# Performance work log

Measured on AMD Instinct MI355X. Metric: run time of the kernel, lower is better.

Reference implementation:

```python
import jax, jax.numpy as jnp
import numpy as np

D_MODEL = 768
NUM_HEADS = 12
D_K = D_MODEL // NUM_HEADS
D_FF = 3072
EPS = 1e-5


def _layer_norm(x, gamma, beta):
    mu = jnp.mean(x, axis=-1, keepdims=True)
    var = jnp.mean(jnp.square(x - mu), axis=-1, keepdims=True)
    return (x - mu) * jax.lax.rsqrt(var + EPS) * gamma + beta


def setup_inputs() -> dict:
    key = jax.random.key(0)
    ks = jax.random.split(key, 16)
    s = 1.0 / np.sqrt(D_MODEL)
    sf = 1.0 / np.sqrt(D_FF)
    inp = {
        "x": jax.random.normal(ks[0], (2, 2048, D_MODEL), dtype=jnp.float32),
        "Wq": jax.random.uniform(ks[1], (D_MODEL, D_MODEL), jnp.float32, -s, s),
        "bq": jax.random.uniform(ks[2], (D_MODEL,), jnp.float32, -s, s),
        "Wk": jax.random.uniform(ks[3], (D_MODEL, D_MODEL), jnp.float32, -s, s),
        "bk": jax.random.uniform(ks[4], (D_MODEL,), jnp.float32, -s, s),
        "Wv": jax.random.uniform(ks[5], (D_MODEL, D_MODEL), jnp.float32, -s, s),
        "bv": jax.random.uniform(ks[6], (D_MODEL,), jnp.float32, -s, s),
        "Wo": jax.random.uniform(ks[7], (D_MODEL, D_MODEL), jnp.float32, -s, s),
        "bo": jax.random.uniform(ks[8], (D_MODEL,), jnp.float32, -s, s),
        "W1": jax.random.uniform(ks[9], (D_MODEL, D_FF), jnp.float32, -s, s),
        "b1": jax.random.uniform(ks[10], (D_FF,), jnp.float32, -s, s),
        "W2": jax.random.uniform(ks[11], (D_FF, D_MODEL), jnp.float32, -sf, sf),
        "b2": jax.random.uniform(ks[12], (D_MODEL,), jnp.float32, -sf, sf),
        "g1": jnp.ones((D_MODEL,), jnp.float32),
        "be1": jnp.zeros((D_MODEL,), jnp.float32),
        "g2": jnp.ones((D_MODEL,), jnp.float32),
        "be2": jnp.zeros((D_MODEL,), jnp.float32),
    }
    return inp


def reference(x, Wq, bq, Wk, bk, Wv, bv, Wo, bo, W1, b1, W2, b2, g1, be1, g2, be2):
    B, S, _ = x.shape

    def split(h):  # (B,S,D) -> (B,H,S,Dk)
        return h.reshape(B, S, NUM_HEADS, D_K).transpose(0, 2, 1, 3)

    q = split(x @ Wq + bq)
    k = split(x @ Wk + bk)
    v = split(x @ Wv + bv)

    # naive attention: materialize full (B,H,S,S) scores as in the original
    scores = jnp.einsum("bhsd,bhtd->bhst", q, k) / np.sqrt(D_K)
    attn = jax.nn.softmax(scores, axis=-1)
    ctx = jnp.einsum("bhst,bhtd->bhsd", attn, v)
    ctx = ctx.transpose(0, 2, 1, 3).reshape(B, S, D_MODEL)
    attn_out = ctx @ Wo + bo

    x = _layer_norm(x + attn_out, g1, be1)
    ff = jax.nn.relu(x @ W1 + b1) @ W2 + b2
    x = _layer_norm(x + ff, g2, be2)
    return x
```

## Files before the change

kernel.cpp:

```cpp
#include <hip/hip_runtime.h>
#include <cstdint>


typedef unsigned short u16;
typedef unsigned int u32;
typedef __attribute__((ext_vector_type(4))) float f32x4;
typedef __attribute__((ext_vector_type(8))) short s16x8;
typedef __attribute__((ext_vector_type(4))) u16  u16x4;
typedef __attribute__((ext_vector_type(2))) u32  u32x2;

#define AS1 __attribute__((address_space(1)))
#define AS3 __attribute__((address_space(3)))

__device__ __forceinline__ u16 f2b(float f) {
  union { float f; unsigned u; } v; v.f = f;
  unsigned r = v.u + 0x7FFFu + ((v.u >> 16) & 1u);
  return (u16)(r >> 16);
}

__device__ __forceinline__ float b2f(u16 v) {
  union { float f; u32 u; } x; x.u = ((u32)v) << 16; return x.f;
}

__device__ __forceinline__ void gl_lds16(const void* g, void* lds_uniform_base) {
  __builtin_amdgcn_global_load_lds((const AS1 void*)g, (AS3 void*)lds_uniform_base, 16, 0, 0);
}

__device__ __forceinline__ f32x4 mfma16(s16x8 a, s16x8 b, f32x4 c) {
  return __builtin_amdgcn_mfma_f32_16x16x32_bf16(a, b, c, 0, 0, 0);
}

__device__ __forceinline__ u32 cvt_pk_bf16(float lo, float hi) {
  u32 r;
  asm("v_cvt_pk_bf16_f32 %0, %1, %2" : "=v"(r) : "v"(lo), "v"(hi));
  return r;
}

__device__ __forceinline__ float max3f(float a, float b, float c) {
  return fmaxf(fmaxf(a, b), c);
}

__global__ __launch_bounds__(256) void prep(
    const float* __restrict__ Wq, const float* __restrict__ Wk,
    const float* __restrict__ Wv, const float* __restrict__ Wo,
    const float* __restrict__ W1, const float* __restrict__ W2,
    const float* __restrict__ bq, const float* __restrict__ bk,
    const float* __restrict__ bv, const float* __restrict__ x,
    u16* __restrict__ Wqkv_t, u16* __restrict__ Wo_t,
    u16* __restrict__ W1_t, u16* __restrict__ W2_t,
    float* __restrict__ bqkv, u16* __restrict__ Xb, int convBlocks) {
  __shared__ float ts[32][33];
  const int bid = blockIdx.x;
  const int tx = threadIdx.x, ty = threadIdx.y;
  if (bid < 6912) {
    const float* W; u16* Wt; int K, N, tile;
    if (bid < 2304) {
      int w = bid / 576; tile = bid - w * 576; K = 768; N = 768;
      W = (w == 0) ? Wq : (w == 1) ? Wk : (w == 2) ? Wv : Wo;
      Wt = (w < 3) ? Wqkv_t + (size_t)w * 768 * 768 : Wo_t;
    } else if (bid < 4608) {
      tile = bid - 2304; K = 768; N = 3072; W = W1; Wt = W1_t;
    } else {
      tile = bid - 4608; K = 3072; N = 768; W = W2; Wt = W2_t;
    }
    int ntx = N >> 5;
    int n0 = (tile % ntx) * 32, k0 = (tile / ntx) * 32;
#pragma unroll
    for (int yy = 0; yy < 32; yy += 8)
      ts[ty + yy][tx] = W[(size_t)(k0 + ty + yy) * N + n0 + tx];
    __syncthreads();
#pragma unroll
    for (int yy = 0; yy < 32; yy += 8)
      Wt[(size_t)(n0 + ty + yy) * K + k0 + tx] = f2b(ts[tx][ty + yy]);
  } else if (bid < 6912 + convBlocks) {
    int t = ty * 32 + tx;
    size_t i = ((size_t)(bid - 6912) * 256 + t) * 4;
    f32x4 v = *(const f32x4*)(x + i);
    u16x4 o;
#pragma unroll
    for (int k = 0; k < 4; ++k) o[k] = f2b(v[k]);
    *(u16x4*)(Xb + i) = o;
  } else {
    int t = ty * 32 + tx;
    int i = (bid - 6912 - convBlocks) * 256 + t;
    if (i < 2304) bqkv[i] = (i < 768) ? bq[i] : (i < 1536) ? bk[i - 768] : bv[i - 1536];
  }
}

__global__ __launch_bounds__(256) void transpose_v(const u16* __restrict__ Vh,
                                                   u16* __restrict__ Vt) {
  __shared__ u16 tile[32][33];
  int bh = blockIdx.z;
  int d0 = blockIdx.x * 32, s0 = blockIdx.y * 32;
  const u16* src = Vh + (size_t)bh * 2048 * 64;
  u16* dst = Vt + (size_t)bh * 64 * 2048;
  int x = threadIdx.x, y = threadIdx.y;
#pragma unroll
  for (int yy = 0; yy < 32; yy += 8)
    tile[y + yy][x] = src[(size_t)(s0 + y + yy) * 64 + d0 + x];
  __syncthreads();
#pragma unroll
  for (int yy = 0; yy < 32; yy += 8)
    dst[(size_t)(d0 + y + yy) * 2048 + s0 + x] = tile[x][y + yy];
}

template <int MODE>
__global__ __launch_bounds__(256) void gemm_bt(const u16* __restrict__ A,
                                               const u16* __restrict__ Bt,
                                               const float* __restrict__ bias,
                                               float* __restrict__ Cf, u16* __restrict__ Cb,
                                               u16* __restrict__ Qo, u16* __restrict__ Ko,
                                               u16* __restrict__ Vo, int M, int N, int K,
                                               int Klen) {
  __shared__ __align__(16) u16 lsA[128 * 64];
  __shared__ __align__(16) u16 lsB[128 * 64];
  const int tid = threadIdx.x;
  const int lane = tid & 63, wave = tid >> 6;
  const int lr = lane & 15, lh = lane >> 4;
  const int wr = wave >> 1, wc = wave & 1;

  int bx, by, bz;
  {
    int nx = gridDim.x, ny = gridDim.y, nz = gridDim.z;
    int total = nx * ny * nz;
    int lin = blockIdx.x + nx * (blockIdx.y + ny * blockIdx.z);
    if ((total & 7) == 0) {
      int key = (lin & 7) * (total >> 3) + (lin >> 3);
      by = key % ny;
      int t2 = key / ny;
      bz = t2 % nz;
      bx = t2 / nz;
    } else {
      bx = blockIdx.x; by = blockIdx.y; bz = blockIdx.z;
    }
  }
  const int m0 = by * 128;
  const int n0 = bx * 128;
  const int kB = bz * Klen;

  f32x4 acc[4][4];
#pragma unroll
  for (int i = 0; i < 4; ++i)
#pragma unroll
    for (int j = 0; j < 4; ++j) acc[i][j] = f32x4{0.f, 0.f, 0.f, 0.f};

  const size_t aBase = (size_t)m0 * K;
  const size_t bBase = (size_t)n0 * K;
  const int srow8 = tid >> 3;
  const int scolE = (((tid & 7) * 16) ^ ((srow8 & 7) << 4)) >> 1;
  const int xk = (lr & 7) << 4;

  for (int kt = kB; kt < kB + Klen; kt += 64) {
#pragma unroll
    for (int i = 0; i < 4; ++i) {
      int row = i * 32 + srow8;
      int ldsOff = i * 4096 + wave * 1024;
      gl_lds16(A + aBase + (size_t)row * K + kt + scolE, (char*)lsA + ldsOff);
      gl_lds16(Bt + bBase + (size_t)row * K + kt + scolE, (char*)lsB + ldsOff);
    }
    __syncthreads();
    const char* baA = (const char*)lsA;
    const char* baB = (const char*)lsB;
#pragma unroll
    for (int ks = 0; ks < 2; ++ks) {
      int cb = (ks * 64 + lh * 16) ^ xk;
      s16x8 a[4], b[4];
#pragma unroll
      for (int i = 0; i < 4; ++i) {
        a[i] = *(const s16x8*)(baA + (wr * 64 + i * 16 + lr) * 128 + cb);
        b[i] = *(const s16x8*)(baB + (wc * 64 + i * 16 + lr) * 128 + cb);
      }
#pragma unroll
      for (int i = 0; i < 4; ++i)
#pragma unroll
        for (int j = 0; j < 4; ++j) acc[i][j] = mfma16(a[i], b[j], acc[i][j]);
    }
    __syncthreads();
  }

  float* CfP = Cf + (size_t)bz * M * N;
#pragma unroll
  for (int i = 0; i < 4; ++i) {
    int growb = m0 + wr * 64 + i * 16 + lh * 4;
#pragma unroll
    for (int j = 0; j < 4; ++j) {
      int col = n0 + wc * 64 + j * 16 + lr;
      float bv = (MODE != 0 || bz == 0) ? bias[col] : 0.f;
#pragma unroll
      for (int q = 0; q < 4; ++q) {
        int grow = growb + q;
        float v = acc[i][j][q] + bv;
        if (MODE == 0) {
          CfP[(size_t)grow * N + col] = v;
        } else if (MODE == 1) {
          Cb[(size_t)grow * N + col] = f2b(fmaxf(v, 0.f));
        } else {
          int sel = col / 768;
          int c2 = col - sel * 768;
          int h = c2 >> 6, d = c2 & 63;
          int b = grow >> 11, s = grow & 2047;
          size_t idx = (((size_t)(b * 12 + h)) * 2048 + s) * 64 + d;
          float vv = (sel == 0) ? v * 0.1803368801f : v;
          u16* dst = (sel == 0) ? Qo : (sel == 1) ? Ko : Vo;
          dst[idx] = f2b(vv);
        }
      }
    }
  }
}

__global__ __launch_bounds__(512) void attn(const u16* __restrict__ Qh,
                                            const u16* __restrict__ Kh,
                                            const u16* __restrict__ Vt,
                                            u16* __restrict__ Opb,
                                            float* __restrict__ ml,
                                            int nbh, int ntile) {
  __shared__ __align__(16) u16 lsK[2][64 * 64];
  __shared__ __align__(16) u16 lsV[2][64 * 64];
  __shared__ __align__(16) u16 lsP[8][16 * 64];
  const int tid = threadIdx.x, lane = tid & 63, wave = tid >> 6;
  const int lr = lane & 15, lh = lane >> 4;

  int bx = blockIdx.x, bh = blockIdx.y, z = blockIdx.z;
  {
    int nz = gridDim.z;
    int total = 16 * nbh * nz;
    if ((total & 7) == 0) {
      int lin = bx + 16 * (bh + nbh * z);
      int nl = (lin & 7) * (total >> 3) + (lin >> 3);
      bx = nl & 15;
      bh = (nl >> 4) % nbh;
      z = nl / (16 * nbh);
    }
  }
  const int q0 = bx * 128 + wave * 16;
  const size_t kvBase = (size_t)bh * 2048 * 64;
  const int tB = z * ntile;

  const int srow = tid >> 3;
  const int scol = (((tid & 7) * 16) ^ ((srow & 7) << 4)) >> 1;
  const u16* kSrcBase = Kh + kvBase + (size_t)srow * 64 + scol;
  const u16* vSrcBase = Vt + kvBase + (size_t)srow * 2048 + scol;

  s16x8 qf[2];
#pragma unroll
  for (int ks = 0; ks < 2; ++ks)
    qf[ks] = *(const s16x8*)(Qh + kvBase + (size_t)(q0 + lr) * 64 + ks * 32 + lh * 8);

  s16x8 onesf;
#pragma unroll
  for (int k = 0; k < 8; ++k) onesf[k] = (short)0x3F80;

  f32x4 oacc[4];
  f32x4 aOnes = f32x4{0.f, 0.f, 0.f, 0.f};
  float mrow = -1e30f;
#pragma unroll
  for (int d = 0; d < 4; ++d) oacc[d] = f32x4{0.f, 0.f, 0.f, 0.f};

  gl_lds16(kSrcBase + (size_t)tB * 4096, (char*)lsK[0] + wave * 1024);
  gl_lds16(vSrcBase + tB * 64,           (char*)lsV[0] + wave * 1024);

  for (int it = 0; it < ntile; ++it) {
    const int cur = it & 1;
    __syncthreads();

    s16x8 kb[2][4];
#pragma unroll
    for (int ks = 0; ks < 2; ++ks)
#pragma unroll
      for (int j = 0; j < 4; ++j) {
        int r = j * 16 + lr;
        kb[ks][j] = *(const s16x8*)((const char*)lsK[cur] + r * 128 +
                                    ((ks * 64 + lh * 16) ^ ((r & 7) << 4)));
      }

    if (it + 1 < ntile) {
      int t = tB + it + 1;
      gl_lds16(kSrcBase + (size_t)t * 4096, (char*)lsK[cur ^ 1] + wave * 1024);
      gl_lds16(vSrcBase + t * 64,           (char*)lsV[cur ^ 1] + wave * 1024);
    }

    f32x4 st[4];
#pragma unroll
    for (int j = 0; j < 4; ++j) st[j] = f32x4{0.f, 0.f, 0.f, 0.f};
    __builtin_amdgcn_s_setprio(1);
#pragma unroll
    for (int ks = 0; ks < 2; ++ks)
#pragma unroll
      for (int j = 0; j < 4; ++j) st[j] = mfma16(kb[ks][j], qf[ks], st[j]);
    __builtin_amdgcn_s_setprio(0);

    float mx;
    {
      float t0 = max3f(st[0][0], st[0][1], st[0][2]);
      float t1 = max3f(st[0][3], st[1][0], st[1][1]);
      float t2 = max3f(st[1][2], st[1][3], st[2][0]);
      float t3 = max3f(st[2][1], st[2][2], st[2][3]);
      float t4 = max3f(st[3][0], st[3][1], st[3][2]);
      mx = fmaxf(max3f(t0, t1, t2), max3f(t3, t4, st[3][3]));
      mx = fmaxf(mx, __shfl_xor(mx, 16));
      mx = fmaxf(mx, __shfl_xor(mx, 32));
    }
    if (__any(mx > mrow + 11.f)) {
      float mn = fmaxf(mrow, mx);
      float al = exp2f(mrow - mn);
      mrow = mn;
#pragma unroll
      for (int q = 0; q < 4; ++q) aOnes[q] *= al;
#pragma unroll
      for (int d = 0; d < 4; ++d)
#pragma unroll
        for (int q = 0; q < 4; ++q) oacc[d][q] *= al;
    }

#pragma unroll
    for (int j = 0; j < 4; ++j) {
      float p0 = exp2f(st[j][0] - mrow);
      float p1 = exp2f(st[j][1] - mrow);
      float p2 = exp2f(st[j][2] - mrow);
      float p3 = exp2f(st[j][3] - mrow);
      u32x2 pk;
      pk.x = cvt_pk_bf16(p0, p1);
      pk.y = cvt_pk_bf16(p2, p3);
      *(u32x2*)((char*)lsP[wave] + lr * 128 + ((j * 32 + lh * 8) ^ ((lr & 7) << 4))) = pk;
    }

    __builtin_amdgcn_s_setprio(1);
#pragma unroll
    for (int ks = 0; ks < 2; ++ks) {
      s16x8 pa = *(const s16x8*)((const char*)lsP[wave] + lr * 128 +
                                 ((ks * 64 + lh * 16) ^ ((lr & 7) << 4)));
      aOnes = mfma16(onesf, pa, aOnes);
#pragma unroll
      for (int d = 0; d < 4; ++d) {
        int r = d * 16 + lr;
        s16x8 vb = *(const s16x8*)((const char*)lsV[cur] + r * 128 +
                                   ((ks * 64 + lh * 16) ^ ((r & 7) << 4)));
        oacc[d] = mfma16(vb, pa, oacc[d]);
      }
    }
    __builtin_amdgcn_s_setprio(0);
  }

  {
    int s = q0 + lr;
    size_t r = ((size_t)z * nbh + bh) * 2048 + s;
#pragma unroll
    for (int d = 0; d < 4; ++d) {
      u32x2 pk;
      pk.x = cvt_pk_bf16(oacc[d][0], oacc[d][1]);
      pk.y = cvt_pk_bf16(oacc[d][2], oacc[d][3]);
      *(u32x2*)(Opb + r * 64 + d * 16 + lh * 4) = pk;
    }
    if (lh == 0) { ml[r * 2] = mrow; ml[r * 2 + 1] = aOnes[0]; }
  }
}

template <int NZ>
__global__ __launch_bounds__(256) void attn_combine(const u16* __restrict__ Opb,
                                                    const float* __restrict__ ml,
                                                    u16* __restrict__ ctx, int nbh) {
  size_t i = (size_t)blockIdx.x * 256 + threadIdx.x;
  int d4 = (int)(i & 15);
  size_t rs = i >> 4;
  size_t zs = (size_t)nbh * 2048;
  float m[NZ], l[NZ];
  float mx = -1e30f;
#pragma unroll
  for (int p = 0; p < NZ; ++p) {
    m[p] = ml[(p * zs + rs) * 2];
    l[p] = ml[(p * zs + rs) * 2 + 1];
    mx = fmaxf(mx, m[p]);
  }
  float wsum = 0.f, a[NZ];
#pragma unroll
  for (int p = 0; p < NZ; ++p) { a[p] = exp2f(m[p] - mx); wsum += l[p] * a[p]; }
  float inv = 1.f / wsum;
  f32x4 o = f32x4{0.f, 0.f, 0.f, 0.f};
#pragma unroll
  for (int p = 0; p < NZ; ++p) {
    u16x4 op = *(const u16x4*)(Opb + (p * zs + rs) * 64 + d4 * 4);
#pragma unroll
    for (int k = 0; k < 4; ++k) o[k] += b2f(op[k]) * a[p];
  }
  int bh = (int)(rs >> 11), s = (int)(rs & 2047);
  int b = bh / 12, h = bh - b * 12;
  u16x4 r;
#pragma unroll
  for (int k = 0; k < 4; ++k) r[k] = f2b(o[k] * inv);
  *(u16x4*)(ctx + ((size_t)(b * 2048 + s)) * 768 + h * 64 + d4 * 4) = r;
}

template <int NP>
__global__ __launch_bounds__(256) void resid_ln(const float* __restrict__ xin,
                                                const float* __restrict__ yp,
                                                size_t pstride,
                                                const float* __restrict__ gamma,
                                                const float* __restrict__ beta,
                                                float* __restrict__ outf,
                                                u16* __restrict__ outb) {
  const int row = blockIdx.x, t = threadIdx.x;
  const size_t base4 = (size_t)row * 192;
  const bool act = t < 192;
  f32x4 v = f32x4{0.f, 0.f, 0.f, 0.f};
  float s = 0.f, s2 = 0.f;
  if (act) {
    v = ((const f32x4*)xin)[base4 + t];
#pragma unroll
    for (int p = 0; p < NP; ++p) {
      f32x4 y = ((const f32x4*)(yp + p * pstride))[base4 + t];
#pragma unroll
      for (int k = 0; k < 4; ++k) v[k] += y[k];
    }
    s = (v[0] + v[1]) + (v[2] + v[3]);
    s2 = (v[0] * v[0] + v[1] * v[1]) + (v[2] * v[2] + v[3] * v[3]);
  }
#pragma unroll
  for (int off = 32; off > 0; off >>= 1) {
    s += __shfl_down(s, off, 64);
    s2 += __shfl_down(s2, off, 64);
  }
  __shared__ float red[8];
  int lane = t & 63, wave = t >> 6;
  if (lane == 0) { red[wave] = s; red[4 + wave] = s2; }
  __syncthreads();
  s = red[0] + red[1] + red[2] + red[3];
  s2 = red[4] + red[5] + red[6] + red[7];
  const float inv = 1.f / 768.f;
  float mu = s * inv;
  float var = fmaxf(s2 * inv - mu * mu, 0.f);
  float rs = rsqrtf(var + 1e-5f);
  if (act) {
    f32x4 g = ((const f32x4*)gamma)[t];
    f32x4 bb = ((const f32x4*)beta)[t];
    f32x4 o;
#pragma unroll
    for (int k = 0; k < 4; ++k) o[k] = (v[k] - mu) * rs * g[k] + bb[k];
    if (outf) ((f32x4*)outf)[base4 + t] = o;
    if (outb) {
      u16x4 ob;
#pragma unroll
      for (int k = 0; k < 4; ++k) ob[k] = f2b(o[k]);
      ((u16x4*)outb)[base4 + t] = ob;
    }
  }
}

extern "C" void kernel_launch(void* const* d_in, const int* in_sizes, int n_in,
                              void* d_out, int out_size, void* d_ws, size_t ws_size,
                              hipStream_t stream) {
  const float* x   = (const float*)d_in[0];
  const float* Wq  = (const float*)d_in[1];
  const float* bq  = (const float*)d_in[2];
  const float* Wk  = (const float*)d_in[3];
  const float* bk  = (const float*)d_in[4];
  const float* Wv  = (const float*)d_in[5];
  const float* bv  = (const float*)d_in[6];
  const float* Wo  = (const float*)d_in[7];
  const float* bo  = (const float*)d_in[8];
  const float* W1  = (const float*)d_in[9];
  const float* b1  = (const float*)d_in[10];
  const float* W2  = (const float*)d_in[11];
  const float* b2  = (const float*)d_in[12];
  const float* g1  = (const float*)d_in[13];
  const float* be1 = (const float*)d_in[14];
  const float* g2  = (const float*)d_in[15];
  const float* be2 = (const float*)d_in[16];
  float* out = (float*)d_out;

  const int M = in_sizes[0] / 768;
  const int B = M / 2048;
  const int nbh = B * 12;

  char* ws = (char*)d_ws;
  size_t off = 0;
  auto alloc = [&](size_t bytes) -> void* {
    void* p = ws + off;
    off += (bytes + 255) & ~(size_t)255;
    return p;
  };
  u16*   Wqkv_t = (u16*)alloc((size_t)2304 * 768 * 2);
  u16*   Wo_t   = (u16*)alloc((size_t)768 * 768 * 2);
  u16*   W1_t   = (u16*)alloc((size_t)3072 * 768 * 2);
  u16*   W2_t   = (u16*)alloc((size_t)768 * 3072 * 2);
  float* bqkv   = (float*)alloc(2304 * 4);
  u16*   Xb     = (u16*)alloc((size_t)M * 768 * 2);
  u16*   Qh     = (u16*)alloc((size_t)M * 768 * 2);
  u16*   Kh     = (u16*)alloc((size_t)M * 768 * 2);
  u16*   Vh     = (u16*)alloc((size_t)M * 768 * 2);
  u16*   Vt     = (u16*)alloc((size_t)M * 768 * 2);

  size_t pstride = (size_t)M * 768;
  size_t fixedRest = pstride * 4  + pstride * 2  +
                     (size_t)M * 3072 * 2  + 4096;
  const int ZSPLIT = 2;
  size_t opElems = (size_t)ZSPLIT * nbh * 2048 * 64;
  size_t attnBytes = opElems * 2 + (size_t)ZSPLIT * nbh * 2048 * 2 * 4;
  size_t reg4 = attnBytes > pstride * 16 ? attnBytes : pstride * 16;
  int FSPLIT;
  size_t regionBytes;
  if (off + reg4 + fixedRest <= ws_size) {
    FSPLIT = 4; regionBytes = reg4;
  } else {
    FSPLIT = 2;
    regionBytes = attnBytes > pstride * 8 ? attnBytes : pstride * 8;
  }
  float* region = (float*)alloc(regionBytes);
  u16*   Opb  = (u16*)region;
  float* ml   = (float*)((char*)region + opElems * 2);
  float* ffnPart  = region;
  float* projPart = (float*)Qh;
  float* x1f  = (float*)alloc(pstride * 4);
  u16*   x1b  = (u16*)alloc(pstride * 2);
  u16*   hb   = (u16*)alloc((size_t)M * 3072 * 2);
  u16*   ctx  = Xb;

  dim3 tb(32, 8);
  const int convBlocks = (M * 768) / 1024;
  prep<<<6912 + convBlocks + 9, tb, 0, stream>>>(
      Wq, Wk, Wv, Wo, W1, W2, bq, bk, bv, x,
      Wqkv_t, Wo_t, W1_t, W2_t, bqkv, Xb, convBlocks);

  gemm_bt<2><<<dim3(2304 / 128, M / 128), 256, 0, stream>>>(
      Xb, Wqkv_t, bqkv, nullptr, nullptr, Qh, Kh, Vh, M, 2304, 768, 768);

  transpose_v<<<dim3(2, 64, nbh), tb, 0, stream>>>(Vh, Vt);

  attn<<<dim3(16, nbh, ZSPLIT), 512, 0, stream>>>(Qh, Kh, Vt, Opb, ml, nbh, 32 / ZSPLIT);
  attn_combine<2><<<nbh * 128, 256, 0, stream>>>(Opb, ml, ctx, nbh);

  gemm_bt<0><<<dim3(768 / 128, M / 128, 2), 256, 0, stream>>>(
      ctx, Wo_t, bo, projPart, nullptr, nullptr, nullptr, nullptr, M, 768, 768, 384);

  resid_ln<2><<<M, 256, 0, stream>>>(x, projPart, pstride, g1, be1, x1f, x1b);

  gemm_bt<1><<<dim3(3072 / 128, M / 128), 256, 0, stream>>>(
      x1b, W1_t, b1, nullptr, hb, nullptr, nullptr, nullptr, M, 3072, 768, 768);

  if (FSPLIT == 4) {
    gemm_bt<0><<<dim3(768 / 128, M / 128, 4), 256, 0, stream>>>(
        hb, W2_t, b2, ffnPart, nullptr, nullptr, nullptr, nullptr, M, 768, 3072, 768);
    resid_ln<4><<<M, 256, 0, stream>>>(x1f, ffnPart, pstride, g2, be2, out, nullptr);
  } else {
    gemm_bt<0><<<dim3(768 / 128, M / 128, 2), 256, 0, stream>>>(
        hb, W2_t, b2, ffnPart, nullptr, nullptr, nullptr, nullptr, M, 768, 3072, 1536);
    resid_ln<2><<<M, 256, 0, stream>>>(x1f, ffnPart, pstride, g2, be2, out, nullptr);
  }
}
```

Before: 213.0 us.

## Double-buffer GEMM LDS tiles to overlap global loads with MFMA

Makes the shared-memory A/B tiles in gemm_bt double-buffered and issues the next K-tile's global-to-LDS loads before computing on the current one. Partial vmcnt waits and raw s_barrier calls replace __syncthreads, so load latency can be hidden behind MFMA work. This doubles LDS use to 64KB per block, which may lower occupancy, and depends on the hand-counted vmcnt value being correct.

```diff
diff --git a/kernel.cpp b/kernel.cpp
--- a/kernel.cpp
+++ b/kernel.cpp
@@ -38,6 +38,12 @@
 
 __device__ __forceinline__ float max3f(float a, float b, float c) {
   return fmaxf(fmaxf(a, b), c);
+}
+
+__device__ __forceinline__ void block_barrier() {
+  asm volatile("" ::: "memory");
+  __builtin_amdgcn_s_barrier();
+  asm volatile("" ::: "memory");
 }
 
 __global__ __launch_bounds__(256) void prep(
@@ -112,8 +118,8 @@
                                                u16* __restrict__ Qo, u16* __restrict__ Ko,
                                                u16* __restrict__ Vo, int M, int N, int K,
                                                int Klen) {
-  __shared__ __align__(16) u16 lsA[128 * 64];
-  __shared__ __align__(16) u16 lsB[128 * 64];
+  __shared__ __align__(16) u16 lsA[2][128 * 64];
+  __shared__ __align__(16) u16 lsB[2][128 * 64];
   const int tid = threadIdx.x;
   const int lane = tid & 63, wave = tid >> 6;
   const int lr = lane & 15, lh = lane >> 4;
@@ -150,17 +156,29 @@
   const int scolE = (((tid & 7) * 16) ^ ((srow8 & 7) << 4)) >> 1;
   const int xk = (lr & 7) << 4;
 
-  for (int kt = kB; kt < kB + Klen; kt += 64) {
+  auto stage = [&](int buf, int kt) {
 #pragma unroll
     for (int i = 0; i < 4; ++i) {
       int row = i * 32 + srow8;
-      int ldsOff = i * 4096 + wave * 1024;
+      int ldsOff = buf * 16384 + i * 4096 + wave * 1024;
       gl_lds16(A + aBase + (size_t)row * K + kt + scolE, (char*)lsA + ldsOff);
       gl_lds16(Bt + bBase + (size_t)row * K + kt + scolE, (char*)lsB + ldsOff);
     }
-    __syncthreads();
-    const char* baA = (const char*)lsA;
-    const char* baB = (const char*)lsB;
+  };
+
+  const int nk = Klen >> 6;
+  stage(0, kB);
+  for (int t = 0; t < nk; ++t) {
+    const int cur = t & 1;
+    if (t + 1 < nk) {
+      stage(cur ^ 1, kB + (t + 1) * 64);
+      asm volatile("s_waitcnt vmcnt(8)" ::: "memory");
+    } else {
+      asm volatile("s_waitcnt vmcnt(0)" ::: "memory");
+    }
+    block_barrier();
+    const char* baA = (const char*)lsA + cur * 16384;
+    const char* baB = (const char*)lsB + cur * 16384;
 #pragma unroll
     for (int ks = 0; ks < 2; ++ks) {
       int cb = (ks * 64 + lh * 16) ^ xk;
@@ -175,7 +193,7 @@
 #pragma unroll
         for (int j = 0; j < 4; ++j) acc[i][j] = mfma16(a[i], b[j], acc[i][j]);
     }
-    __syncthreads();
+    block_barrier();
   }
 
   float* CfP = Cf + (size_t)bz * M * N;
```

Result: no change. 210.6 us (-1.1%).
